# Kernel tuning notes

Measured on AMD Instinct MI355X. Metric: run time of the kernel, lower is better.

The kernel has to match this reference:

```python
import jax, jax.numpy as jnp
import numpy as np

EPS = 1e-8

def setup_inputs() -> dict:
    key = jax.random.key(0)
    k1, k2, k3, k4, k5 = jax.random.split(key, 5)
    B, S, d, H = 4, 1024, 512, 8
    hd = d // H
    x = jax.random.normal(k1, (B, S, d), dtype=jnp.float32)
    V = jax.random.normal(k2, (B, S, H, hd), dtype=jnp.float32)
    # binary biological mask [B, S, S]
    M = (jax.random.uniform(k3, (B, S, S)) > 0.5).astype(jnp.float32)
    in_proj_w = jax.random.normal(k4, (3 * d, d), dtype=jnp.float32) * 0.02
    in_proj_b = jnp.zeros((3 * d,), dtype=jnp.float32)
    out_w = jax.random.normal(k5, (d, d), dtype=jnp.float32) * 0.02
    out_b = jnp.zeros((d,), dtype=jnp.float32)
    return {"x": x, "V": V, "M": M, "in_proj_w": in_proj_w,
            "in_proj_b": in_proj_b, "out_w": out_w, "out_b": out_b}


def reference(x, V, M, in_proj_w, in_proj_b, out_w, out_b):
    B, S, d = x.shape
    H, hd = V.shape[2], V.shape[3]
    # packed QKV projection (torch MHA in_proj); V slice is computed by torch
    # but its result is discarded, so only Q,K slices influence the output.
    qkv = x @ in_proj_w.T + in_proj_b            # [B, S, 3d]
    q = qkv[..., :d].reshape(B, S, H, hd).transpose(0, 2, 1, 3)        # [B,H,S,hd]
    k = qkv[..., d:2 * d].reshape(B, S, H, hd).transpose(0, 2, 1, 3)   # [B,H,S,hd]
    scores = jnp.einsum("bhqd,bhkd->bhqk", q, k) / jnp.sqrt(jnp.float32(hd))
    A = jax.nn.softmax(scores, axis=-1)           # [B,H,S,S] per-head attn weights
    # biological mask + L1 renormalization (post-hoc, as in original)
    A_sparse = A * M[:, None, :, :]
    norm = jnp.sum(jnp.abs(A_sparse), axis=-1, keepdims=True) + EPS
    A_bar = A_sparse / norm
    # custom V: [B,S,H,hd] -> [B,H,S,hd]
    Vp = V.transpose(0, 2, 1, 3)
    out = jnp.einsum("bhqk,bhkd->bhqd", A_bar, Vp)  # [B,H,S,hd]
    out = out.transpose(0, 2, 1, 3).reshape(B, S, d)
    return out @ out_w.T + out_b
```

## Files before the change

### kernel.cpp

```cpp
#include <hip/hip_runtime.h>
#include <hip/hip_bf16.h>

#define BB 4
#define SS 1024
#define DD 512
#define HH 8
#define HD 64

typedef __attribute__((ext_vector_type(8))) short bf16x8;
typedef __attribute__((ext_vector_type(4))) float f32x4;

static __device__ __forceinline__ unsigned short f2b(float f) {
  union { float f; unsigned int u; } c; c.f = f;
  return (unsigned short)((c.u + 0x7fffu + ((c.u >> 16) & 1u)) >> 16);
}

static __device__ __forceinline__ unsigned cvtpk(float lo, float hi) {
  unsigned r;
  asm("v_cvt_pk_bf16_f32 %0, %1, %2" : "=v"(r) : "v"(lo), "v"(hi));
  return r;
}

__global__ __launch_bounds__(256) void prep(
    const float* __restrict__ x, const float* __restrict__ W1,
    const float* __restrict__ Wo, const float* __restrict__ Mmask,
    const float* __restrict__ V, unsigned short* __restrict__ xb,
    unsigned short* __restrict__ W1b, unsigned short* __restrict__ Wob,
    unsigned char* __restrict__ Mpack, unsigned short* __restrict__ Vt) {
  __shared__ float Ls[64][65];
  const int bid = blockIdx.x;
  const int tid = threadIdx.x;

  if (bid < 1408) {
    const float* src; unsigned short* dst; size_t off;
    if (bid < 1024) { src = x;  dst = xb;  off = ((size_t)bid * 256 + tid) * 8; }
    else if (bid < 1280) { src = W1; dst = W1b; off = ((size_t)(bid - 1024) * 256 + tid) * 8; }
    else { src = Wo; dst = Wob; off = ((size_t)(bid - 1280) * 256 + tid) * 8; }
    const float4 a = *(const float4*)(src + off);
    const float4 b = *(const float4*)(src + off + 4);
    union { unsigned short s[8]; uint4 v; } o;
    o.s[0] = f2b(a.x); o.s[1] = f2b(a.y); o.s[2] = f2b(a.z); o.s[3] = f2b(a.w);
    o.s[4] = f2b(b.x); o.s[5] = f2b(b.y); o.s[6] = f2b(b.z); o.s[7] = f2b(b.w);
    *(uint4*)(dst + off) = o.v;
  } else if (bid < 3456) {
    const size_t g = (size_t)(bid - 1408) * 256 + tid;
    const float4 a = *(const float4*)(Mmask + g * 8);
    const float4 b = *(const float4*)(Mmask + g * 8 + 4);
    unsigned v = 0;
    v |= (a.x > 0.5f) ? 1u : 0u;   v |= (a.y > 0.5f) ? 2u : 0u;
    v |= (a.z > 0.5f) ? 4u : 0u;   v |= (a.w > 0.5f) ? 8u : 0u;
    v |= (b.x > 0.5f) ? 16u : 0u;  v |= (b.y > 0.5f) ? 32u : 0u;
    v |= (b.z > 0.5f) ? 64u : 0u;  v |= (b.w > 0.5f) ? 128u : 0u;
    Mpack[g] = (unsigned char)v;
  } else {
    const int id = bid - 3456;
    const int s0 = (id & 15) * 64, h = (id >> 4) & 7, b = id >> 7;
    {
      const int r = tid >> 2, cs = (tid & 3) * 16;
      const float* src = V + ((size_t)((b * SS + s0 + r) * HH) + h) * HD + cs;
#pragma unroll
      for (int j = 0; j < 4; j++) {
        const float4 v = *(const float4*)(src + j * 4);
        Ls[r][cs + j * 4 + 0] = v.x; Ls[r][cs + j * 4 + 1] = v.y;
        Ls[r][cs + j * 4 + 2] = v.z; Ls[r][cs + j * 4 + 3] = v.w;
      }
    }
    __syncthreads();
    {
      const int d = tid >> 2, ss = (tid & 3) * 16;
      union { unsigned short s[16]; uint4 v[2]; } o;
#pragma unroll
      for (int j = 0; j < 16; j++) o.s[j] = f2b(Ls[ss + j][d]);
      unsigned short* dst =
          Vt + ((size_t)((b * HH + h) * HD + d)) * SS + s0 + ss;
      *(uint4*)dst = o.v[0];
      *(uint4*)(dst + 8) = o.v[1];
    }
  }
}

__global__ __launch_bounds__(256) void gemm_qk(
    const unsigned short* __restrict__ xb, const unsigned short* __restrict__ W1b,
    const float* __restrict__ bias, unsigned short* __restrict__ qkb) {
  __shared__ unsigned short As[128][40];
  __shared__ unsigned short Bs[64][40];
  const int tid = threadIdx.x;
  const int lane = tid & 63, wave = tid >> 6;
  const int l16 = lane & 15, quad = lane >> 4;
  const int row0 = blockIdx.y * 128, col0 = blockIdx.x * 64;

  f32x4 acc[2][4];
#pragma unroll
  for (int i = 0; i < 2; i++)
#pragma unroll
    for (int j = 0; j < 4; j++) acc[i][j] = (f32x4){0.f, 0.f, 0.f, 0.f};

  const int ra = tid >> 1, csa = (tid & 1) * 16;
  const int rb = tid >> 2, csb = (tid & 3) * 8;
  const unsigned short* ap = xb + (size_t)(row0 + ra) * DD + csa;
  const unsigned short* bp = W1b + (size_t)(col0 + rb) * DD + csb;

  uint4 pa0 = *(const uint4*)ap, pa1 = *(const uint4*)(ap + 8);
  uint4 pb = *(const uint4*)bp;

  for (int k0 = 0; k0 < DD; k0 += 32) {
    __syncthreads();
    *(uint4*)&As[ra][csa] = pa0;
    *(uint4*)&As[ra][csa + 8] = pa1;
    *(uint4*)&Bs[rb][csb] = pb;
    __syncthreads();
    if (k0 + 32 < DD) {
      pa0 = *(const uint4*)(ap + k0 + 32);
      pa1 = *(const uint4*)(ap + k0 + 40);
      pb = *(const uint4*)(bp + k0 + 32);
    }

    const bf16x8 a0 = *(const bf16x8*)&As[wave * 32 + l16][quad * 8];
    const bf16x8 a1 = *(const bf16x8*)&As[wave * 32 + 16 + l16][quad * 8];
#pragma unroll
    for (int nt = 0; nt < 4; nt++) {
      const bf16x8 bb = *(const bf16x8*)&Bs[nt * 16 + l16][quad * 8];
      acc[0][nt] = __builtin_amdgcn_mfma_f32_16x16x32_bf16(a0, bb, acc[0][nt], 0, 0, 0);
      acc[1][nt] = __builtin_amdgcn_mfma_f32_16x16x32_bf16(a1, bb, acc[1][nt], 0, 0, 0);
    }
  }

#pragma unroll
  for (int nt = 0; nt < 4; nt++) {
    const int col = col0 + nt * 16 + l16;
    const float bv = bias[col];
    const float scale = (col < DD) ? 0.125f : 1.0f;
#pragma unroll
    for (int mi = 0; mi < 2; mi++)
#pragma unroll
      for (int reg = 0; reg < 4; reg++) {
        const int row = row0 + wave * 32 + mi * 16 + quad * 4 + reg;
        qkb[(size_t)row * 1024 + col] = f2b((acc[mi][nt][reg] + bv) * scale);
      }
  }
}

__global__ __launch_bounds__(256) void gemm_out(
    const unsigned short* __restrict__ Ab, const unsigned short* __restrict__ Wob,
    const float* __restrict__ bias, float* __restrict__ out) {
  __shared__ unsigned short As[64][40];
  __shared__ unsigned short Bs[64][40];
  const int tid = threadIdx.x;
  const int lane = tid & 63, wave = tid >> 6;
  const int l16 = lane & 15, quad = lane >> 4;
  const int row0 = blockIdx.y * 64, col0 = blockIdx.x * 64;

  f32x4 acc[4];
#pragma unroll
  for (int j = 0; j < 4; j++) acc[j] = (f32x4){0.f, 0.f, 0.f, 0.f};

  const int r = tid >> 2, cs = (tid & 3) * 8;
  const unsigned short* ap = Ab + (size_t)(row0 + r) * DD + cs;
  const unsigned short* bp = Wob + (size_t)(col0 + r) * DD + cs;

  uint4 pa = *(const uint4*)ap;
  uint4 pb = *(const uint4*)bp;

  for (int k0 = 0; k0 < DD; k0 += 32) {
    __syncthreads();
    *(uint4*)&As[r][cs] = pa;
    *(uint4*)&Bs[r][cs] = pb;
    __syncthreads();
    if (k0 + 32 < DD) {
      pa = *(const uint4*)(ap + k0 + 32);
      pb = *(const uint4*)(bp + k0 + 32);
    }

    const bf16x8 a0 = *(const bf16x8*)&As[wave * 16 + l16][quad * 8];
#pragma unroll
    for (int nt = 0; nt < 4; nt++) {
      const bf16x8 bb = *(const bf16x8*)&Bs[nt * 16 + l16][quad * 8];
      acc[nt] = __builtin_amdgcn_mfma_f32_16x16x32_bf16(a0, bb, acc[nt], 0, 0, 0);
    }
  }

#pragma unroll
  for (int nt = 0; nt < 4; nt++) {
    const int col = col0 + nt * 16 + l16;
    const float bv = bias[col];
#pragma unroll
    for (int reg = 0; reg < 4; reg++) {
      const int row = row0 + wave * 16 + quad * 4 + reg;
      out[(size_t)row * DD + col] = acc[nt][reg] + bv;
    }
  }
}

__global__ __launch_bounds__(512, 4) void flash_attn_fused(
    const unsigned short* __restrict__ qkb, const unsigned short* __restrict__ Vt,
    const unsigned char* __restrict__ Mpack, unsigned short* __restrict__ attnb) {
  __shared__ unsigned short QP[64][72];
  __shared__ unsigned short P2[64][72];
  __shared__ unsigned short Ks[2][64][72];
  __shared__ unsigned short Vs[2][64][72];
  __shared__ float SmS[2][64];

  const int tid = threadIdx.x;
  const int lane = tid & 63, wave = tid >> 6;
  const int l16 = lane & 15, quad = lane >> 4;
  const int wq = wave & 3, sp = wave >> 2;

  const int g = blockIdx.x;
  const int xcd = g & 7, loc = g >> 3;
  const int gr = xcd + 8 * (loc >> 4);
  const int q0 = (loc & 15) * 64;
  const int h = gr & 7;
  const int b = gr >> 3;

  const int r2 = tid >> 3, cs2 = (tid & 7) * 8;

  {
    const unsigned short* s = qkb + (size_t)(b * SS + q0 + r2) * 1024 + h * HD + cs2;
    *(uint4*)&QP[r2][cs2] = *(const uint4*)s;
  }

  const unsigned char* mp =
      Mpack + (size_t)(b * SS + q0 + wq * 16 + l16) * 128 + sp * 64;
  uint2 pm = *(const uint2*)mp;

  __syncthreads();
  const bf16x8 bQ0 = *(const bf16x8*)&QP[wq * 16 + l16][quad * 8];
  const bf16x8 bQ1 = *(const bf16x8*)&QP[wq * 16 + l16][32 + quad * 8];
  unsigned short(*Ps)[72] =
      (unsigned short(*)[72])(sp ? &P2[wq * 16][0] : &QP[wq * 16][0]);

  float Smp = 0.f;
  f32x4 O[4];
#pragma unroll
  for (int i = 0; i < 4; i++) O[i] = (f32x4){0.f, 0.f, 0.f, 0.f};

  const unsigned short* kp0 =
      qkb + (size_t)(b * SS + r2) * 1024 + DD + h * HD + cs2;
  const unsigned short* kp1 = kp0 + (size_t)512 * 1024;
  const unsigned short* vp0 =
      Vt + ((size_t)((b * HH + h) * HD + r2)) * SS + cs2;
  const unsigned short* vp1 = vp0 + 512;

  uint4 pk0 = *(const uint4*)kp0, pk1 = *(const uint4*)kp1;
  uint4 pv0 = *(const uint4*)vp0, pv1 = *(const uint4*)vp1;

#pragma unroll
  for (int i = 0; i < 8; i++) {
    __syncthreads();
    *(uint4*)&Ks[0][r2][cs2] = pk0;
    *(uint4*)&Ks[1][r2][cs2] = pk1;
    *(uint4*)&Vs[0][r2][cs2] = pv0;
    *(uint4*)&Vs[1][r2][cs2] = pv1;
    __syncthreads();

    const uint2 pm_cur = pm;
    if (i < 7) {
      pk0 = *(const uint4*)(kp0 + (size_t)(i + 1) * 64 * 1024);
      pk1 = *(const uint4*)(kp1 + (size_t)(i + 1) * 64 * 1024);
      pv0 = *(const uint4*)(vp0 + (i + 1) * 64);
      pv1 = *(const uint4*)(vp1 + (i + 1) * 64);
      pm = *(const uint2*)(mp + (i + 1) * 8);
    }

#pragma unroll
    for (int t = 0; t < 4; t++) {
      const bf16x8 aK0 = *(const bf16x8*)&Ks[sp][t * 16 + l16][quad * 8];
      const bf16x8 aK1 = *(const bf16x8*)&Ks[sp][t * 16 + l16][32 + quad * 8];
      f32x4 a = (f32x4){0.f, 0.f, 0.f, 0.f};
      a = __builtin_amdgcn_mfma_f32_16x16x32_bf16(aK0, bQ0, a, 0, 0, 0);
      a = __builtin_amdgcn_mfma_f32_16x16x32_bf16(aK1, bQ1, a, 0, 0, 0);
      const unsigned nib =
          ((t < 2 ? pm_cur.x : pm_cur.y) >> ((t & 1) * 16 + quad * 4)) & 0xFu;
      float e0 = __expf(a[0]); e0 = (nib & 1u) ? e0 : 0.f;
      float e1 = __expf(a[1]); e1 = (nib & 2u) ? e1 : 0.f;
      float e2 = __expf(a[2]); e2 = (nib & 4u) ? e2 : 0.f;
      float e3 = __expf(a[3]); e3 = (nib & 8u) ? e3 : 0.f;
      Smp += (e0 + e1) + (e2 + e3);
      uint2 w;
      w.x = cvtpk(e0, e1);
      w.y = cvtpk(e2, e3);
      *(uint2*)&Ps[l16][t * 16 + quad * 4] = w;
    }

    const bf16x8 aP0 = *(const bf16x8*)&Ps[l16][quad * 8];
    const bf16x8 aP1 = *(const bf16x8*)&Ps[l16][32 + quad * 8];
#pragma unroll
    for (int dt = 0; dt < 4; dt++) {
      const bf16x8 bV0 = *(const bf16x8*)&Vs[sp][dt * 16 + l16][quad * 8];
      const bf16x8 bV1 = *(const bf16x8*)&Vs[sp][dt * 16 + l16][32 + quad * 8];
      O[dt] = __builtin_amdgcn_mfma_f32_16x16x32_bf16(aP0, bV0, O[dt], 0, 0, 0);
      O[dt] = __builtin_amdgcn_mfma_f32_16x16x32_bf16(aP1, bV1, O[dt], 0, 0, 0);
    }
  }

  Smp += __shfl_xor(Smp, 16);
  Smp += __shfl_xor(Smp, 32);
  if (lane < 16) SmS[sp][wq * 16 + lane] = Smp;

  __syncthreads();
  float* Of = reinterpret_cast<float*>(&Ks[0][0][0]);
  if (sp == 1) {
#pragma unroll
    for (int dt = 0; dt < 4; dt++)
#pragma unroll
      for (int reg = 0; reg < 4; reg++)
        Of[(wq * 16 + quad * 4 + reg) * 64 + dt * 16 + l16] = O[dt][reg];
  }
  __syncthreads();

  if (sp == 0) {
    float inv[4];
#pragma unroll
    for (int reg = 0; reg < 4; reg++) {
      const int ql = wq * 16 + quad * 4 + reg;
      inv[reg] = 1.0f / (SmS[0][ql] + SmS[1][ql] + 1e-12f);
    }
#pragma unroll
    for (int dt = 0; dt < 4; dt++)
#pragma unroll
      for (int reg = 0; reg < 4; reg++) {
        const int ql = wq * 16 + quad * 4 + reg;
        const float v = (O[dt][reg] + Of[ql * 64 + dt * 16 + l16]) * inv[reg];
        attnb[(size_t)(b * SS + q0 + ql) * DD + h * HD + dt * 16 + l16] = f2b(v);
      }
  }
}

extern "C" void kernel_launch(void* const* d_in, const int* in_sizes, int n_in,
                              void* d_out, int out_size, void* d_ws,
                              size_t ws_size, hipStream_t stream) {
  const float* x = (const float*)d_in[0];
  const float* V = (const float*)d_in[1];
  const float* Mmask = (const float*)d_in[2];
  const float* in_proj_w = (const float*)d_in[3];
  const float* in_proj_b = (const float*)d_in[4];
  const float* out_w = (const float*)d_in[5];
  const float* out_b = (const float*)d_in[6];
  float* out = (float*)d_out;

  unsigned char* ws = (unsigned char*)d_ws;
  unsigned short* qkb   = (unsigned short*)(ws);
  unsigned short* xb    = (unsigned short*)(ws + (8ull << 20));
  unsigned short* W1b   = (unsigned short*)(ws + (12ull << 20));
  unsigned short* Wob   = (unsigned short*)(ws + (13ull << 20));
  unsigned short* Vt    = (unsigned short*)(ws + (14ull << 20));
  unsigned short* attnb = (unsigned short*)(ws + (18ull << 20));
  unsigned char*  Mpack = ws + (38ull << 20) + (256u << 10);

  prep<<<3968, 256, 0, stream>>>(x, in_proj_w, out_w, Mmask, V,
                                 xb, W1b, Wob, Mpack, Vt);
  gemm_qk<<<dim3(16, 32), 256, 0, stream>>>(xb, W1b, in_proj_b, qkb);
  flash_attn_fused<<<512, 512, 0, stream>>>(qkb, Vt, Mpack, attnb);
  gemm_out<<<dim3(8, 64), 256, 0, stream>>>(attnb, Wob, out_b, out);
}
```

Baseline: 130.7 us.

## Double-buffer K tiles in LDS and read V fragments directly from global

The kernel now double-buffers K tiles in shared memory: the next tile is stored into the alternate buffer while the current one is consumed, which leaves one barrier per iteration instead of two. V is no longer staged through LDS. Each wave loads its MFMA B-operand fragments for V directly from global memory, which frees LDS and cuts LDS traffic. In exchange, V reads become per-wave global loads with some redundancy across waves, and each wave may stall on global latency right before its PV MFMAs.

```diff
diff --git a/kernel.cpp b/kernel.cpp
--- a/kernel.cpp
+++ b/kernel.cpp
@@ -196,8 +196,7 @@
     const unsigned char* __restrict__ Mpack, unsigned short* __restrict__ attnb) {
   __shared__ unsigned short QP[64][72];
   __shared__ unsigned short P2[64][72];
-  __shared__ unsigned short Ks[2][64][72];
-  __shared__ unsigned short Vs[2][64][72];
+  __shared__ unsigned short Ks[2][2][64][72];
   __shared__ float SmS[2][64];
 
   const int tid = threadIdx.x;
@@ -223,6 +222,22 @@
       Mpack + (size_t)(b * SS + q0 + wq * 16 + l16) * 128 + sp * 64;
   uint2 pm = *(const uint2*)mp;
 
+  const unsigned short* kp0 =
+      qkb + (size_t)(b * SS + r2) * 1024 + DD + h * HD + cs2;
+  const unsigned short* kp1 = kp0 + (size_t)512 * 1024;
+
+  const unsigned short* vb =
+      Vt + ((size_t)((b * HH + h) * HD + l16)) * SS + sp * 512 + quad * 8;
+
+  {
+    const uint4 t0k0 = *(const uint4*)kp0;
+    const uint4 t0k1 = *(const uint4*)kp1;
+    *(uint4*)&Ks[0][0][r2][cs2] = t0k0;
+    *(uint4*)&Ks[0][1][r2][cs2] = t0k1;
+  }
+  uint4 pk0 = *(const uint4*)(kp0 + (size_t)64 * 1024);
+  uint4 pk1 = *(const uint4*)(kp1 + (size_t)64 * 1024);
+
   __syncthreads();
   const bf16x8 bQ0 = *(const bf16x8*)&QP[wq * 16 + l16][quad * 8];
   const bf16x8 bQ1 = *(const bf16x8*)&QP[wq * 16 + l16][32 + quad * 8];
@@ -234,38 +249,25 @@
 #pragma unroll
   for (int i = 0; i < 4; i++) O[i] = (f32x4){0.f, 0.f, 0.f, 0.f};
 
-  const unsigned short* kp0 =
-      qkb + (size_t)(b * SS + r2) * 1024 + DD + h * HD + cs2;
-  const unsigned short* kp1 = kp0 + (size_t)512 * 1024;
-  const unsigned short* vp0 =
-      Vt + ((size_t)((b * HH + h) * HD + r2)) * SS + cs2;
-  const unsigned short* vp1 = vp0 + 512;
-
-  uint4 pk0 = *(const uint4*)kp0, pk1 = *(const uint4*)kp1;
-  uint4 pv0 = *(const uint4*)vp0, pv1 = *(const uint4*)vp1;
-
 #pragma unroll
   for (int i = 0; i < 8; i++) {
-    __syncthreads();
-    *(uint4*)&Ks[0][r2][cs2] = pk0;
-    *(uint4*)&Ks[1][r2][cs2] = pk1;
-    *(uint4*)&Vs[0][r2][cs2] = pv0;
-    *(uint4*)&Vs[1][r2][cs2] = pv1;
-    __syncthreads();
-
+    const int cur = i & 1, nxt = cur ^ 1;
     const uint2 pm_cur = pm;
+
     if (i < 7) {
-      pk0 = *(const uint4*)(kp0 + (size_t)(i + 1) * 64 * 1024);
-      pk1 = *(const uint4*)(kp1 + (size_t)(i + 1) * 64 * 1024);
-      pv0 = *(const uint4*)(vp0 + (i + 1) * 64);
-      pv1 = *(const uint4*)(vp1 + (i + 1) * 64);
+      *(uint4*)&Ks[nxt][0][r2][cs2] = pk0;
+      *(uint4*)&Ks[nxt][1][r2][cs2] = pk1;
+      if (i < 6) {
+        pk0 = *(const uint4*)(kp0 + (size_t)(i + 2) * 64 * 1024);
+        pk1 = *(const uint4*)(kp1 + (size_t)(i + 2) * 64 * 1024);
+      }
       pm = *(const uint2*)(mp + (i + 1) * 8);
     }
 
 #pragma unroll
     for (int t = 0; t < 4; t++) {
-      const bf16x8 aK0 = *(const bf16x8*)&Ks[sp][t * 16 + l16][quad * 8];
-      const bf16x8 aK1 = *(const bf16x8*)&Ks[sp][t * 16 + l16][32 + quad * 8];
+      const bf16x8 aK0 = *(const bf16x8*)&Ks[cur][sp][t * 16 + l16][quad * 8];
+      const bf16x8 aK1 = *(const bf16x8*)&Ks[cur][sp][t * 16 + l16][32 + quad * 8];
       f32x4 a = (f32x4){0.f, 0.f, 0.f, 0.f};
       a = __builtin_amdgcn_mfma_f32_16x16x32_bf16(aK0, bQ0, a, 0, 0, 0);
       a = __builtin_amdgcn_mfma_f32_16x16x32_bf16(aK1, bQ1, a, 0, 0, 0);
@@ -286,11 +288,14 @@
     const bf16x8 aP1 = *(const bf16x8*)&Ps[l16][32 + quad * 8];
 #pragma unroll
     for (int dt = 0; dt < 4; dt++) {
-      const bf16x8 bV0 = *(const bf16x8*)&Vs[sp][dt * 16 + l16][quad * 8];
-      const bf16x8 bV1 = *(const bf16x8*)&Vs[sp][dt * 16 + l16][32 + quad * 8];
+      const unsigned short* vt = vb + (size_t)(dt * 16) * SS + i * 64;
+      const bf16x8 bV0 = *(const bf16x8*)vt;
+      const bf16x8 bV1 = *(const bf16x8*)(vt + 32);
       O[dt] = __builtin_amdgcn_mfma_f32_16x16x32_bf16(aP0, bV0, O[dt], 0, 0, 0);
       O[dt] = __builtin_amdgcn_mfma_f32_16x16x32_bf16(aP1, bV1, O[dt], 0, 0, 0);
     }
+
+    __syncthreads();
   }
 
   Smp += __shfl_xor(Smp, 16);
@@ -298,7 +303,7 @@
   if (lane < 16) SmS[sp][wq * 16 + lane] = Smp;
 
   __syncthreads();
-  float* Of = reinterpret_cast<float*>(&Ks[0][0][0]);
+  float* Of = reinterpret_cast<float*>(&Ks[0][0][0][0]);
   if (sp == 1) {
 #pragma unroll
     for (int dt = 0; dt < 4; dt++)
```

After: 150.7 us. 1.15x slower.
